# Optimization experiments

Measured on AMD Instinct MI355X. Metric: run time of the kernel, lower is better.

Reference implementation:

```python
import jax, jax.numpy as jnp
import numpy as np

N_NODES = 100000
N_EDGES = 1600000
NFEAT = 256
NHID = 128
NCLASS = 8


def setup_inputs() -> dict:
    key = jax.random.key(0)
    k1, k2, k3, k4, k5 = jax.random.split(key, 5)
    x = jax.random.normal(k1, (N_NODES, NFEAT), dtype=jnp.float32)
    edge_index = jax.random.randint(k2, (2, N_EDGES), 0, N_NODES, dtype=jnp.int64)
    # GCNConv weight (glorot) and bias
    s1 = float(np.sqrt(6.0 / (NFEAT + NHID)))
    W1 = jax.random.uniform(k3, (NFEAT, NHID), dtype=jnp.float32, minval=-s1, maxval=s1)
    b1 = jnp.zeros((NHID,), dtype=jnp.float32)
    # fc Linear (xavier uniform per weights_init, bias zero)
    s2 = float(np.sqrt(6.0 / (NHID + NCLASS)))
    Wfc = jax.random.uniform(k4, (NHID, NCLASS), dtype=jnp.float32, minval=-s2, maxval=s2)
    bfc = jnp.zeros((NCLASS,), dtype=jnp.float32)
    return {"x": x, "edge_index": edge_index, "W1": W1, "b1": b1, "Wfc": Wfc, "bfc": bfc}


def gcn_conv(x, src, dst, W, b, n_nodes):
    # PyG GCNConv: h = X W; out_i = sum_j norm_ij * h_j over A+I with sym norm
    h = x @ W  # [N, nhid]
    deg = jax.ops.segment_sum(jnp.ones_like(dst, dtype=h.dtype), dst, num_segments=n_nodes)
    dinv = jnp.where(deg > 0, jax.lax.rsqrt(deg), 0.0)  # deg^{-1/2}
    norm = dinv[src] * dinv[dst]  # [E+N]
    msg = h[src] * norm[:, None]  # gather + scale, [E+N, nhid]
    out = jax.ops.segment_sum(msg, dst, num_segments=n_nodes)
    return out + b


def reference(x, edge_index, W1, b1, Wfc, bfc):
    n = x.shape[0]
    loop = jnp.arange(n, dtype=edge_index.dtype)
    src = jnp.concatenate([edge_index[0], loop])  # add self-loops
    dst = jnp.concatenate([edge_index[1], loop])
    h = gcn_conv(x, src, dst, W1, b1, n)  # GCN_Body (no activation in forward)
    return h @ Wfc + bfc  # fc
```

## Files before the change

kernel.cpp:

```cpp
#include <hip/hip_runtime.h>

#define N_NODES 100000
#define NFEAT 256
#define NHID 128
#define NCLASS 8

#define BSH 8
#define BUCK 256
#define NBUCK ((N_NODES + BUCK - 1) / BUCK)
#define VX 8
#define CAPS 704
#define GSTRIDE (NBUCK * CAPS)
#define CAPB (CAPS * VX)
#define NBLK1 2048
#define OVF_CAP 32768

__global__ __launch_bounds__(512) void init_kernel(const float* __restrict__ W1,
        const float* __restrict__ b1, const float* __restrict__ Wfc,
        const float* __restrict__ bfc, float* __restrict__ Wf,
        float* __restrict__ cvec, int* __restrict__ gcur, int* __restrict__ ovf_cnt) {
    int tid = threadIdx.x;
    if (blockIdx.x == 0) {
        __shared__ float wfs[NHID * NCLASS];
        __shared__ float bs[NHID];
        for (int i = tid; i < NHID * NCLASS; i += 512) wfs[i] = Wfc[i];
        if (tid < NHID) bs[tid] = b1[tid];
        __syncthreads();
        if (tid < NFEAT) {
            float acc[NCLASS] = {};
            for (int h = 0; h < NHID; h++) {
                float w = W1[tid * NHID + h];
                #pragma unroll
                for (int c = 0; c < NCLASS; c++) acc[c] += w * wfs[h * NCLASS + c];
            }
            #pragma unroll
            for (int c = 0; c < NCLASS; c++) Wf[tid * NCLASS + c] = acc[c];
        }
        if (tid < NCLASS) {
            float a = bfc[tid];
            for (int h = 0; h < NHID; h++) a += bs[h] * wfs[h * NCLASS + tid];
            cvec[tid] = a;
        }
    } else {
        int i = (blockIdx.x - 1) * 512 + tid;
        if (i < VX * NBUCK) {
            int g = i / NBUCK;
            int b = i - g * NBUCK;
            gcur[i] = g * GSTRIDE + b * CAPS;
        }
        if (blockIdx.x == 1 && tid == 0) *ovf_cnt = 0;
    }
}

__global__ __launch_bounds__(256) void scat_kernel(const int* __restrict__ esrc,
        const int* __restrict__ edst, int* __restrict__ gcur,
        int* __restrict__ ebufP, int* __restrict__ ovf_cnt,
        int* __restrict__ ovfbuf, int chunk, int nE) {
    __shared__ int h[NBUCK];
    __shared__ int lcur[NBUCK];
    int tid = threadIdx.x;
    int xcc;
    asm volatile("s_getreg_b32 %0, hwreg(HW_REG_XCC_ID)" : "=s"(xcc));
    xcc &= (VX - 1);
    for (int i = tid; i < NBUCK; i += 256) h[i] = 0;
    __syncthreads();
    int e0 = blockIdx.x * chunk;
    int e1 = min(e0 + chunk, nE);
    for (int e = e0 + tid * 4; e + 3 < e1; e += 1024) {
        int4 d = *(const int4*)&edst[e];
        atomicAdd(&h[d.x >> BSH], 1); atomicAdd(&h[d.y >> BSH], 1);
        atomicAdd(&h[d.z >> BSH], 1); atomicAdd(&h[d.w >> BSH], 1);
    }
    int full = e0 + ((e1 - e0) & ~3);
    if (full + tid < e1) atomicAdd(&h[edst[full + tid] >> BSH], 1);
    __syncthreads();
    const int gbase = xcc * GSTRIDE;
    for (int b = tid; b < NBUCK; b += 256) {
        int c = h[b];
        lcur[b] = c ? atomicAdd(&gcur[xcc * NBUCK + b], c) : 0;
    }
    __syncthreads();
    for (int e = e0 + tid * 4; e + 3 < e1; e += 1024) {
        int4 s = *(const int4*)&esrc[e];
        int4 d = *(const int4*)&edst[e];
        int b0 = d.x >> BSH, b1_ = d.y >> BSH, b2 = d.z >> BSH, b3 = d.w >> BSH;
        int p0 = atomicAdd(&lcur[b0], 1);
        int p1 = atomicAdd(&lcur[b1_], 1);
        int p2 = atomicAdd(&lcur[b2], 1);
        int p3 = atomicAdd(&lcur[b3], 1);
        int k0 = (s.x << BSH) | (d.x & (BUCK - 1));
        int k1 = (s.y << BSH) | (d.y & (BUCK - 1));
        int k2 = (s.z << BSH) | (d.z & (BUCK - 1));
        int k3 = (s.w << BSH) | (d.w & (BUCK - 1));
        if (p0 < gbase + b0 * CAPS + CAPS) ebufP[p0] = k0;
        else { int op = atomicAdd(ovf_cnt, 1); if (op < OVF_CAP) { ovfbuf[2*op] = k0; ovfbuf[2*op+1] = b0; } }
        if (p1 < gbase + b1_ * CAPS + CAPS) ebufP[p1] = k1;
        else { int op = atomicAdd(ovf_cnt, 1); if (op < OVF_CAP) { ovfbuf[2*op] = k1; ovfbuf[2*op+1] = b1_; } }
        if (p2 < gbase + b2 * CAPS + CAPS) ebufP[p2] = k2;
        else { int op = atomicAdd(ovf_cnt, 1); if (op < OVF_CAP) { ovfbuf[2*op] = k2; ovfbuf[2*op+1] = b2; } }
        if (p3 < gbase + b3 * CAPS + CAPS) ebufP[p3] = k3;
        else { int op = atomicAdd(ovf_cnt, 1); if (op < OVF_CAP) { ovfbuf[2*op] = k3; ovfbuf[2*op+1] = b3; } }
    }
    if (full + tid < e1) {
        int s = esrc[full + tid], d = edst[full + tid];
        int b = d >> BSH;
        int p = atomicAdd(&lcur[b], 1);
        int k = (s << BSH) | (d & (BUCK - 1));
        if (p < gbase + b * CAPS + CAPS) ebufP[p] = k;
        else { int op = atomicAdd(ovf_cnt, 1); if (op < OVF_CAP) { ovfbuf[2*op] = k; ovfbuf[2*op+1] = b; } }
    }
}

__global__ __launch_bounds__(512) void deg_dinv_kernel(const int* __restrict__ ebufP,
        const int* __restrict__ gcur, const int* __restrict__ ovf_cnt,
        const int* __restrict__ ovfbuf, float* __restrict__ dinv) {
    __shared__ int cnt[BUCK];
    int b = blockIdx.x, tid = threadIdx.x;
    if (tid < BUCK) cnt[tid] = 0;
    __syncthreads();
    #pragma unroll
    for (int g = 0; g < VX; g++) {
        int base = g * GSTRIDE + b * CAPS;
        int end = min(gcur[g * NBUCK + b], base + CAPS);
        int n = end - base;
        const int4* p4 = (const int4*)&ebufP[base];
        int n4 = n >> 2;
        for (int k = tid; k < n4; k += 512) {
            int4 p = p4[k];
            atomicAdd(&cnt[p.x & (BUCK - 1)], 1);
            atomicAdd(&cnt[p.y & (BUCK - 1)], 1);
            atomicAdd(&cnt[p.z & (BUCK - 1)], 1);
            atomicAdd(&cnt[p.w & (BUCK - 1)], 1);
        }
        for (int k = (n4 << 2) + tid; k < n; k += 512)
            atomicAdd(&cnt[ebufP[base + k] & (BUCK - 1)], 1);
    }
    int nov = min(*ovf_cnt, OVF_CAP);
    for (int i = tid; i < nov; i += 512)
        if (ovfbuf[2 * i + 1] == b) atomicAdd(&cnt[ovfbuf[2 * i] & (BUCK - 1)], 1);
    __syncthreads();
    if (tid < BUCK) {
        int node = (b << BSH) + tid;
        if (node < N_NODES) dinv[node] = rsqrtf((float)(cnt[tid] + 1));
    }
}

__global__ __launch_bounds__(64) void z_kernel(const float* __restrict__ X,
                                               const float* __restrict__ Wf,
                                               const float* __restrict__ dinv,
                                               float* __restrict__ Zs, int n) {
    int row = blockIdx.x * 64 + threadIdx.x;
    bool ok = row < n;
    int r = ok ? row : n - 1;
    const float4* xr = (const float4*)(X + (long)r * NFEAT);
    float dv = dinv[r];
    float acc[NCLASS] = {};
    #pragma unroll 8
    for (int k = 0; k < 64; k++) {
        float4 x4 = xr[k];
        const float* w = Wf + k * 32;
        #pragma unroll
        for (int c = 0; c < NCLASS; c++)
            acc[c] += x4.x * w[c] + x4.y * w[8 + c]
                    + x4.z * w[16 + c] + x4.w * w[24 + c];
    }
    if (ok) {
        float4 o0, o1;
        o0.x = acc[0] * dv; o0.y = acc[1] * dv; o0.z = acc[2] * dv; o0.w = acc[3] * dv;
        o1.x = acc[4] * dv; o1.y = acc[5] * dv; o1.z = acc[6] * dv; o1.w = acc[7] * dv;
        ((float4*)Zs)[(long)row * 2]     = o0;
        ((float4*)Zs)[(long)row * 2 + 1] = o1;
    }
}

__global__ __launch_bounds__(512) void sort_gather_kernel(
        const float* __restrict__ Zs,
        const int* __restrict__ ebufP,
        const int* __restrict__ gcur,
        const int* __restrict__ ovf_cnt,
        const int* __restrict__ ovfbuf,
        const float* __restrict__ cvec,
        float* __restrict__ out, int n) {
    __shared__ int cnt[BUCK];
    __shared__ int off[BUCK + 1];
    __shared__ int ss[BUCK];
    __shared__ int sorted[CAPB];
    int b = blockIdx.x, tid = threadIdx.x;
    const float4* Zs4 = (const float4*)Zs;
    float4 c0v = ((const float4*)cvec)[0];
    float4 c1v = ((const float4*)cvec)[1];
    int nov = min(*ovf_cnt, OVF_CAP);

    if (tid < BUCK) cnt[tid] = 0;
    __syncthreads();
    #pragma unroll
    for (int g = 0; g < VX; g++) {
        int base = g * GSTRIDE + b * CAPS;
        int end = min(gcur[g * NBUCK + b], base + CAPS);
        int nn = end - base;
        const int4* p4 = (const int4*)&ebufP[base];
        int n4 = nn >> 2;
        for (int k = tid; k < n4; k += 512) {
            int4 p = p4[k];
            atomicAdd(&cnt[p.x & (BUCK - 1)], 1);
            atomicAdd(&cnt[p.y & (BUCK - 1)], 1);
            atomicAdd(&cnt[p.z & (BUCK - 1)], 1);
            atomicAdd(&cnt[p.w & (BUCK - 1)], 1);
        }
        for (int k = (n4 << 2) + tid; k < nn; k += 512)
            atomicAdd(&cnt[ebufP[base + k] & (BUCK - 1)], 1);
    }
    for (int i = tid; i < nov; i += 512)
        if (ovfbuf[2 * i + 1] == b) atomicAdd(&cnt[ovfbuf[2 * i] & (BUCK - 1)], 1);
    __syncthreads();

    int t = (tid < BUCK) ? cnt[tid] : 0;
    if (tid < BUCK) ss[tid] = t;
    __syncthreads();
    for (int o = 1; o < BUCK; o <<= 1) {
        int u = 0;
        if (tid < BUCK && tid >= o) u = ss[tid - o];
        __syncthreads();
        if (tid < BUCK) ss[tid] += u;
        __syncthreads();
    }
    if (tid < BUCK) {
        off[tid] = ss[tid] - t;
        cnt[tid] = ss[tid] - t;
        if (tid == BUCK - 1) off[BUCK] = ss[tid];
    }
    __syncthreads();

    #pragma unroll
    for (int g = 0; g < VX; g++) {
        int base = g * GSTRIDE + b * CAPS;
        int end = min(gcur[g * NBUCK + b], base + CAPS);
        int nn = end - base;
        const int4* p4 = (const int4*)&ebufP[base];
        int n4 = nn >> 2;
        for (int k = tid; k < n4; k += 512) {
            int4 p = p4[k];
            int s0 = atomicAdd(&cnt[p.x & (BUCK - 1)], 1);
            int s1 = atomicAdd(&cnt[p.y & (BUCK - 1)], 1);
            int s2 = atomicAdd(&cnt[p.z & (BUCK - 1)], 1);
            int s3 = atomicAdd(&cnt[p.w & (BUCK - 1)], 1);
            sorted[s0] = p.x >> BSH;
            sorted[s1] = p.y >> BSH;
            sorted[s2] = p.z >> BSH;
            sorted[s3] = p.w >> BSH;
        }
        for (int k = (n4 << 2) + tid; k < nn; k += 512) {
            int p = ebufP[base + k];
            int slot = atomicAdd(&cnt[p & (BUCK - 1)], 1);
            sorted[slot] = p >> BSH;
        }
    }
    for (int i = tid; i < nov; i += 512) {
        if (ovfbuf[2 * i + 1] == b) {
            int p = ovfbuf[2 * i];
            int slot = atomicAdd(&cnt[p & (BUCK - 1)], 1);
            sorted[slot] = p >> BSH;
        }
    }
    __syncthreads();

    int li = tid >> 1;
    int hh = tid & 1;
    int node = (b << BSH) + li;
    if (node < n) {
        int k0 = off[li], k1 = off[li + 1];
        float4 a = Zs4[node * 2 + hh];
        int k = k0;
        for (; k + 1 < k1; k += 2) {
            int s0 = sorted[k], s1 = sorted[k + 1];
            float4 z0 = Zs4[s0 * 2 + hh];
            float4 z1 = Zs4[s1 * 2 + hh];
            a.x += z0.x + z1.x; a.y += z0.y + z1.y;
            a.z += z0.z + z1.z; a.w += z0.w + z1.w;
        }
        if (k < k1) {
            float4 z = Zs4[sorted[k] * 2 + hh];
            a.x += z.x; a.y += z.y; a.z += z.z; a.w += z.w;
        }
        float dd = rsqrtf((float)(k1 - k0 + 1));
        float4 cv = hh ? c1v : c0v;
        float4 o;
        o.x = a.x * dd + cv.x; o.y = a.y * dd + cv.y;
        o.z = a.z * dd + cv.z; o.w = a.w * dd + cv.w;
        ((float4*)out)[node * 2 + hh] = o;
    }
}

extern "C" void kernel_launch(void* const* d_in, const int* in_sizes, int n_in,
                              void* d_out, int out_size, void* d_ws, size_t ws_size,
                              hipStream_t stream) {
    const float* x    = (const float*)d_in[0];
    const int*   eidx = (const int*)d_in[1];
    const float* W1   = (const float*)d_in[2];
    const float* b1   = (const float*)d_in[3];
    const float* Wfc  = (const float*)d_in[4];
    const float* bfc  = (const float*)d_in[5];
    float* out = (float*)d_out;

    const int N = N_NODES;
    const int E = in_sizes[1] / 2;

    const int* esrc = eidx;
    const int* edst = eidx + E;

    float* Zs     = (float*)d_ws;
    float* cvec   = Zs + (long)8 * N;
    float* Wf     = cvec + 8;
    float* dinv   = Wf + NFEAT * NCLASS;
    int*   gcur   = (int*)(dinv + N);
    int*   ovfc   = gcur + VX * NBUCK;
    int*   ovfbuf = ovfc + 4;
    int*   ebufP  = ovfbuf + 2 * OVF_CAP;

    const int chunk = (((E + NBLK1 - 1) / NBLK1) + 3) & ~3;

    init_kernel<<<1 + (VX * NBUCK + 511) / 512, 512, 0, stream>>>(
        W1, b1, Wfc, bfc, Wf, cvec, gcur, ovfc);
    scat_kernel<<<NBLK1, 256, 0, stream>>>(esrc, edst, gcur, ebufP, ovfc, ovfbuf, chunk, E);
    deg_dinv_kernel<<<NBUCK, 512, 0, stream>>>(ebufP, gcur, ovfc, ovfbuf, dinv);
    z_kernel<<<(N + 63) / 64, 64, 0, stream>>>(x, Wf, dinv, Zs, N);
    sort_gather_kernel<<<NBUCK, 512, 0, stream>>>(Zs, ebufP, gcur, ovfc, ovfbuf, cvec, out, N);
}
```

Baseline: 230.3 us.

## Fuse X·Wf projection into scatter kernel and apply source dinv in gather

The dense projection Z = X·Wf no longer depends on dinv, so it now runs as extra blocks inside the edge scatter kernel and overlaps the memory-bound X read with the atomic-heavy bucketing. The separate z_kernel launch goes away. In exchange, the gather loop loads dinv[src] per edge and scales each neighbor term, which adds a random 4-byte load per edge, and the self term is now scaled explicitly. The Z blocks come first in the grid, so they may delay the scatter blocks rather than truly overlapping with them.

After: 219.8 us. 1.05x faster.

```diff
diff --git a/kernel.cpp b/kernel.cpp
--- a/kernel.cpp
+++ b/kernel.cpp
@@ -13,6 +13,7 @@
 #define GSTRIDE (NBUCK * CAPS)
 #define CAPB (CAPS * VX)
 #define NBLK1 2048
+#define ZBLKS ((N_NODES + 255) / 256)
 #define OVF_CAP 32768
 
 __global__ __launch_bounds__(512) void init_kernel(const float* __restrict__ W1,
@@ -52,62 +53,90 @@
     }
 }
 
-__global__ __launch_bounds__(256) void scat_kernel(const int* __restrict__ esrc,
+__global__ __launch_bounds__(256) void scat_z_kernel(const int* __restrict__ esrc,
         const int* __restrict__ edst, int* __restrict__ gcur,
         int* __restrict__ ebufP, int* __restrict__ ovf_cnt,
-        int* __restrict__ ovfbuf, int chunk, int nE) {
+        int* __restrict__ ovfbuf,
+        const float* __restrict__ X, const float* __restrict__ Wf,
+        float* __restrict__ Zs, int chunk, int nE, int n) {
     __shared__ int h[NBUCK];
     __shared__ int lcur[NBUCK];
     int tid = threadIdx.x;
-    int xcc;
-    asm volatile("s_getreg_b32 %0, hwreg(HW_REG_XCC_ID)" : "=s"(xcc));
-    xcc &= (VX - 1);
-    for (int i = tid; i < NBUCK; i += 256) h[i] = 0;
-    __syncthreads();
-    int e0 = blockIdx.x * chunk;
-    int e1 = min(e0 + chunk, nE);
-    for (int e = e0 + tid * 4; e + 3 < e1; e += 1024) {
-        int4 d = *(const int4*)&edst[e];
-        atomicAdd(&h[d.x >> BSH], 1); atomicAdd(&h[d.y >> BSH], 1);
-        atomicAdd(&h[d.z >> BSH], 1); atomicAdd(&h[d.w >> BSH], 1);
-    }
-    int full = e0 + ((e1 - e0) & ~3);
-    if (full + tid < e1) atomicAdd(&h[edst[full + tid] >> BSH], 1);
-    __syncthreads();
-    const int gbase = xcc * GSTRIDE;
-    for (int b = tid; b < NBUCK; b += 256) {
-        int c = h[b];
-        lcur[b] = c ? atomicAdd(&gcur[xcc * NBUCK + b], c) : 0;
-    }
-    __syncthreads();
-    for (int e = e0 + tid * 4; e + 3 < e1; e += 1024) {
-        int4 s = *(const int4*)&esrc[e];
-        int4 d = *(const int4*)&edst[e];
-        int b0 = d.x >> BSH, b1_ = d.y >> BSH, b2 = d.z >> BSH, b3 = d.w >> BSH;
-        int p0 = atomicAdd(&lcur[b0], 1);
-        int p1 = atomicAdd(&lcur[b1_], 1);
-        int p2 = atomicAdd(&lcur[b2], 1);
-        int p3 = atomicAdd(&lcur[b3], 1);
-        int k0 = (s.x << BSH) | (d.x & (BUCK - 1));
-        int k1 = (s.y << BSH) | (d.y & (BUCK - 1));
-        int k2 = (s.z << BSH) | (d.z & (BUCK - 1));
-        int k3 = (s.w << BSH) | (d.w & (BUCK - 1));
-        if (p0 < gbase + b0 * CAPS + CAPS) ebufP[p0] = k0;
-        else { int op = atomicAdd(ovf_cnt, 1); if (op < OVF_CAP) { ovfbuf[2*op] = k0; ovfbuf[2*op+1] = b0; } }
-        if (p1 < gbase + b1_ * CAPS + CAPS) ebufP[p1] = k1;
-        else { int op = atomicAdd(ovf_cnt, 1); if (op < OVF_CAP) { ovfbuf[2*op] = k1; ovfbuf[2*op+1] = b1_; } }
-        if (p2 < gbase + b2 * CAPS + CAPS) ebufP[p2] = k2;
-        else { int op = atomicAdd(ovf_cnt, 1); if (op < OVF_CAP) { ovfbuf[2*op] = k2; ovfbuf[2*op+1] = b2; } }
-        if (p3 < gbase + b3 * CAPS + CAPS) ebufP[p3] = k3;
-        else { int op = atomicAdd(ovf_cnt, 1); if (op < OVF_CAP) { ovfbuf[2*op] = k3; ovfbuf[2*op+1] = b3; } }
-    }
-    if (full + tid < e1) {
-        int s = esrc[full + tid], d = edst[full + tid];
-        int b = d >> BSH;
-        int p = atomicAdd(&lcur[b], 1);
-        int k = (s << BSH) | (d & (BUCK - 1));
-        if (p < gbase + b * CAPS + CAPS) ebufP[p] = k;
-        else { int op = atomicAdd(ovf_cnt, 1); if (op < OVF_CAP) { ovfbuf[2*op] = k; ovfbuf[2*op+1] = b; } }
+
+    if (blockIdx.x < ZBLKS) {
+        int row = blockIdx.x * 256 + tid;
+        bool ok = row < n;
+        int r = ok ? row : n - 1;
+        const float4* xr = (const float4*)(X + (long)r * NFEAT);
+        float acc[NCLASS] = {};
+        #pragma unroll 8
+        for (int k = 0; k < 64; k++) {
+            float4 x4 = xr[k];
+            const float* w = Wf + k * 32;
+            #pragma unroll
+            for (int c = 0; c < NCLASS; c++)
+                acc[c] += x4.x * w[c] + x4.y * w[8 + c]
+                        + x4.z * w[16 + c] + x4.w * w[24 + c];
+        }
+        if (ok) {
+            float4 o0, o1;
+            o0.x = acc[0]; o0.y = acc[1]; o0.z = acc[2]; o0.w = acc[3];
+            o1.x = acc[4]; o1.y = acc[5]; o1.z = acc[6]; o1.w = acc[7];
+            ((float4*)Zs)[(long)row * 2]     = o0;
+            ((float4*)Zs)[(long)row * 2 + 1] = o1;
+        }
+    } else {
+        int bid = blockIdx.x - ZBLKS;
+        int xcc;
+        asm volatile("s_getreg_b32 %0, hwreg(HW_REG_XCC_ID)" : "=s"(xcc));
+        xcc &= (VX - 1);
+        for (int i = tid; i < NBUCK; i += 256) h[i] = 0;
+        __syncthreads();
+        int e0 = bid * chunk;
+        int e1 = min(e0 + chunk, nE);
+        for (int e = e0 + tid * 4; e + 3 < e1; e += 1024) {
+            int4 d = *(const int4*)&edst[e];
+            atomicAdd(&h[d.x >> BSH], 1); atomicAdd(&h[d.y >> BSH], 1);
+            atomicAdd(&h[d.z >> BSH], 1); atomicAdd(&h[d.w >> BSH], 1);
+        }
+        int full = e0 + ((e1 - e0) & ~3);
+        if (full + tid < e1) atomicAdd(&h[edst[full + tid] >> BSH], 1);
+        __syncthreads();
+        const int gbase = xcc * GSTRIDE;
+        for (int b = tid; b < NBUCK; b += 256) {
+            int c = h[b];
+            lcur[b] = c ? atomicAdd(&gcur[xcc * NBUCK + b], c) : 0;
+        }
+        __syncthreads();
+        for (int e = e0 + tid * 4; e + 3 < e1; e += 1024) {
+            int4 s = *(const int4*)&esrc[e];
+            int4 d = *(const int4*)&edst[e];
+            int b0 = d.x >> BSH, b1_ = d.y >> BSH, b2 = d.z >> BSH, b3 = d.w >> BSH;
+            int p0 = atomicAdd(&lcur[b0], 1);
+            int p1 = atomicAdd(&lcur[b1_], 1);
+            int p2 = atomicAdd(&lcur[b2], 1);
+            int p3 = atomicAdd(&lcur[b3], 1);
+            int k0 = (s.x << BSH) | (d.x & (BUCK - 1));
+            int k1 = (s.y << BSH) | (d.y & (BUCK - 1));
+            int k2 = (s.z << BSH) | (d.z & (BUCK - 1));
+            int k3 = (s.w << BSH) | (d.w & (BUCK - 1));
+            if (p0 < gbase + b0 * CAPS + CAPS) ebufP[p0] = k0;
+            else { int op = atomicAdd(ovf_cnt, 1); if (op < OVF_CAP) { ovfbuf[2*op] = k0; ovfbuf[2*op+1] = b0; } }
+            if (p1 < gbase + b1_ * CAPS + CAPS) ebufP[p1] = k1;
+            else { int op = atomicAdd(ovf_cnt, 1); if (op < OVF_CAP) { ovfbuf[2*op] = k1; ovfbuf[2*op+1] = b1_; } }
+            if (p2 < gbase + b2 * CAPS + CAPS) ebufP[p2] = k2;
+            else { int op = atomicAdd(ovf_cnt, 1); if (op < OVF_CAP) { ovfbuf[2*op] = k2; ovfbuf[2*op+1] = b2; } }
+            if (p3 < gbase + b3 * CAPS + CAPS) ebufP[p3] = k3;
+            else { int op = atomicAdd(ovf_cnt, 1); if (op < OVF_CAP) { ovfbuf[2*op] = k3; ovfbuf[2*op+1] = b3; } }
+        }
+        if (full + tid < e1) {
+            int s = esrc[full + tid], d = edst[full + tid];
+            int b = d >> BSH;
+            int p = atomicAdd(&lcur[b], 1);
+            int k = (s << BSH) | (d & (BUCK - 1));
+            if (p < gbase + b * CAPS + CAPS) ebufP[p] = k;
+            else { int op = atomicAdd(ovf_cnt, 1); if (op < OVF_CAP) { ovfbuf[2*op] = k; ovfbuf[2*op+1] = b; } }
+        }
     }
 }
 
@@ -145,40 +174,13 @@
     }
 }
 
-__global__ __launch_bounds__(64) void z_kernel(const float* __restrict__ X,
-                                               const float* __restrict__ Wf,
-                                               const float* __restrict__ dinv,
-                                               float* __restrict__ Zs, int n) {
-    int row = blockIdx.x * 64 + threadIdx.x;
-    bool ok = row < n;
-    int r = ok ? row : n - 1;
-    const float4* xr = (const float4*)(X + (long)r * NFEAT);
-    float dv = dinv[r];
-    float acc[NCLASS] = {};
-    #pragma unroll 8
-    for (int k = 0; k < 64; k++) {
-        float4 x4 = xr[k];
-        const float* w = Wf + k * 32;
-        #pragma unroll
-        for (int c = 0; c < NCLASS; c++)
-            acc[c] += x4.x * w[c] + x4.y * w[8 + c]
-                    + x4.z * w[16 + c] + x4.w * w[24 + c];
-    }
-    if (ok) {
-        float4 o0, o1;
-        o0.x = acc[0] * dv; o0.y = acc[1] * dv; o0.z = acc[2] * dv; o0.w = acc[3] * dv;
-        o1.x = acc[4] * dv; o1.y = acc[5] * dv; o1.z = acc[6] * dv; o1.w = acc[7] * dv;
-        ((float4*)Zs)[(long)row * 2]     = o0;
-        ((float4*)Zs)[(long)row * 2 + 1] = o1;
-    }
-}
-
 __global__ __launch_bounds__(512) void sort_gather_kernel(
         const float* __restrict__ Zs,
         const int* __restrict__ ebufP,
         const int* __restrict__ gcur,
         const int* __restrict__ ovf_cnt,
         const int* __restrict__ ovfbuf,
+        const float* __restrict__ dinv,
         const float* __restrict__ cvec,
         float* __restrict__ out, int n) {
     __shared__ int cnt[BUCK];
@@ -269,20 +271,26 @@
     int node = (b << BSH) + li;
     if (node < n) {
         int k0 = off[li], k1 = off[li + 1];
-        float4 a = Zs4[node * 2 + hh];
+        float4 a; a.x = 0.f; a.y = 0.f; a.z = 0.f; a.w = 0.f;
         int k = k0;
         for (; k + 1 < k1; k += 2) {
             int s0 = sorted[k], s1 = sorted[k + 1];
+            float dv0 = dinv[s0], dv1 = dinv[s1];
             float4 z0 = Zs4[s0 * 2 + hh];
             float4 z1 = Zs4[s1 * 2 + hh];
-            a.x += z0.x + z1.x; a.y += z0.y + z1.y;
-            a.z += z0.z + z1.z; a.w += z0.w + z1.w;
+            a.x += dv0 * z0.x + dv1 * z1.x; a.y += dv0 * z0.y + dv1 * z1.y;
+            a.z += dv0 * z0.z + dv1 * z1.z; a.w += dv0 * z0.w + dv1 * z1.w;
         }
         if (k < k1) {
-            float4 z = Zs4[sorted[k] * 2 + hh];
-            a.x += z.x; a.y += z.y; a.z += z.z; a.w += z.w;
+            int s = sorted[k];
+            float dv = dinv[s];
+            float4 z = Zs4[s * 2 + hh];
+            a.x += dv * z.x; a.y += dv * z.y; a.z += dv * z.z; a.w += dv * z.w;
         }
         float dd = rsqrtf((float)(k1 - k0 + 1));
+        float4 zs = Zs4[node * 2 + hh];
+        a.x += dd * zs.x; a.y += dd * zs.y;
+        a.z += dd * zs.z; a.w += dd * zs.w;
         float4 cv = hh ? c1v : c0v;
         float4 o;
         o.x = a.x * dd + cv.x; o.y = a.y * dd + cv.y;
@@ -321,8 +329,8 @@
 
     init_kernel<<<1 + (VX * NBUCK + 511) / 512, 512, 0, stream>>>(
         W1, b1, Wfc, bfc, Wf, cvec, gcur, ovfc);
-    scat_kernel<<<NBLK1, 256, 0, stream>>>(esrc, edst, gcur, ebufP, ovfc, ovfbuf, chunk, E);
+    scat_z_kernel<<<ZBLKS + NBLK1, 256, 0, stream>>>(
+        esrc, edst, gcur, ebufP, ovfc, ovfbuf, x, Wf, Zs, chunk, E, N);
     deg_dinv_kernel<<<NBUCK, 512, 0, stream>>>(ebufP, gcur, ovfc, ovfbuf, dinv);
-    z_kernel<<<(N + 63) / 64, 64, 0, stream>>>(x, Wf, dinv, Zs, N);
-    sort_gather_kernel<<<NBUCK, 512, 0, stream>>>(Zs, ebufP, gcur, ovfc, ovfbuf, cvec, out, N);
-}
+    sort_gather_kernel<<<NBUCK, 512, 0, stream>>>(Zs, ebufP, gcur, ovfc, ovfbuf, dinv, cvec, out, N);
+}
```
